# Optimization experiments

Hardware: AMD Instinct MI355X
Metric: run time of the kernel (lower is better)

The kernel has to match this reference:

```python
import jax, jax.numpy as jnp
import numpy as np

N_NODES = 100000
N_EDGES = 1600000
D = 64
PROP_STEP = 4
RESIDUAL = 1.0


def setup_inputs() -> dict:
    key = jax.random.key(0)
    ks = jax.random.split(key, 6)
    in_feat = jax.random.normal(ks[0], (N_NODES, D), dtype=jnp.float32)
    edge_weight = jax.random.uniform(ks[1], (N_EDGES,), dtype=jnp.float32)
    W1 = jax.random.normal(ks[2], (D, D), dtype=jnp.float32) / np.sqrt(D)
    b1 = jnp.zeros((D,), dtype=jnp.float32)
    W2 = jax.random.normal(ks[3], (D, D), dtype=jnp.float32) / np.sqrt(D)
    b2 = jnp.zeros((D,), dtype=jnp.float32)
    src = jax.random.randint(ks[4], (N_EDGES,), 0, N_NODES, dtype=jnp.int64 if jax.config.jax_enable_x64 else jnp.int32)
    dst = jax.random.randint(ks[5], (N_EDGES,), 0, N_NODES, dtype=jnp.int64 if jax.config.jax_enable_x64 else jnp.int32)
    return {"in_feat": in_feat, "edge_weight": edge_weight, "W1": W1, "b1": b1,
            "W2": W2, "b2": b2, "src": src, "dst": dst}


def _gcn_conv(x, W, b, src, dst, w):
    # GCNConv: out = A_hat @ (x W) + b, A_hat given as weighted edge list
    xw = x @ W                         # [N, D] dense GEMM (small D)
    msg = xw[src] * w[:, None]         # [E, D] gather + scale
    agg = jax.ops.segment_sum(msg, dst, num_segments=N_NODES)  # scatter-add
    return agg + b


def reference(in_feat, edge_weight, W1, b1, W2, b2, src, dst):
    ori = in_feat
    h = _gcn_conv(in_feat, W1, b1, src, dst, edge_weight) + RESIDUAL * ori
    for _ in range(1, PROP_STEP):
        h = _gcn_conv(h, W2, b2, src, dst, edge_weight) + RESIDUAL * ori
    return h
```

## Files before the change

### kernel.cpp

```cpp
#include <hip/hip_runtime.h>
#include <hip/hip_fp16.h>

#define NN 100000
#define NE 1600000
#define D 64
#define NPS 256
#define NS ((NN + NPS - 1) / NPS)
#define CAPS 4608
#define P1_BLOCKS 512
#define P1_CH (NE / P1_BLOCKS)

typedef __attribute__((ext_vector_type(8))) _Float16 half8;
typedef __attribute__((ext_vector_type(4))) _Float16 half4_t;
typedef __attribute__((ext_vector_type(4))) float f32x4;

__global__ void __launch_bounds__(256) gemm64_f32(const float* __restrict__ x,
                                                  const float* __restrict__ W,
                                                  __half* __restrict__ out,
                                                  __half* __restrict__ xh, int n) {
    __shared__ _Float16 sWT[64][72];
    int tid = threadIdx.x;
    for (int i = tid; i < 64 * 64; i += 256) {
        int k = i >> 6, c = i & 63;
        sWT[c][k] = (_Float16)W[i];
    }
    __syncthreads();
    int lane = tid & 63;
    int wid  = tid >> 6;
    int lrow = lane & 15;
    int kslc = lane >> 4;

    half8 bfrag[4][2];
#pragma unroll
    for (int t = 0; t < 4; ++t)
#pragma unroll
        for (int kb = 0; kb < 2; ++kb)
            bfrag[t][kb] = *(const half8*)&sWT[t * 16 + lrow][kb * 32 + kslc * 8];

    int nstrips = (n + 15) >> 4;
    for (int s = blockIdx.x * 4 + wid; s < nstrips; s += gridDim.x * 4) {
        int row = s * 16 + lrow;
        half8 a0 = {}, a1 = {};
        if (row < n) {
            const float* p = x + (size_t)row * 64 + kslc * 8;
            float4 u0 = *(const float4*)p;
            float4 u1 = *(const float4*)(p + 4);
            float4 u2 = *(const float4*)(p + 32);
            float4 u3 = *(const float4*)(p + 36);
            a0 = (half8){(_Float16)u0.x, (_Float16)u0.y, (_Float16)u0.z, (_Float16)u0.w,
                         (_Float16)u1.x, (_Float16)u1.y, (_Float16)u1.z, (_Float16)u1.w};
            a1 = (half8){(_Float16)u2.x, (_Float16)u2.y, (_Float16)u2.z, (_Float16)u2.w,
                         (_Float16)u3.x, (_Float16)u3.y, (_Float16)u3.z, (_Float16)u3.w};
            *(half8*)(xh + (size_t)row * 64 + kslc * 8) = a0;
            *(half8*)(xh + (size_t)row * 64 + 32 + kslc * 8) = a1;
        }
        f32x4 acc0 = {0.f, 0.f, 0.f, 0.f}, acc1 = acc0, acc2 = acc0, acc3 = acc0;
        acc0 = __builtin_amdgcn_mfma_f32_16x16x32_f16(a0, bfrag[0][0], acc0, 0, 0, 0);
        acc0 = __builtin_amdgcn_mfma_f32_16x16x32_f16(a1, bfrag[0][1], acc0, 0, 0, 0);
        acc1 = __builtin_amdgcn_mfma_f32_16x16x32_f16(a0, bfrag[1][0], acc1, 0, 0, 0);
        acc1 = __builtin_amdgcn_mfma_f32_16x16x32_f16(a1, bfrag[1][1], acc1, 0, 0, 0);
        acc2 = __builtin_amdgcn_mfma_f32_16x16x32_f16(a0, bfrag[2][0], acc2, 0, 0, 0);
        acc2 = __builtin_amdgcn_mfma_f32_16x16x32_f16(a1, bfrag[2][1], acc2, 0, 0, 0);
        acc3 = __builtin_amdgcn_mfma_f32_16x16x32_f16(a0, bfrag[3][0], acc3, 0, 0, 0);
        acc3 = __builtin_amdgcn_mfma_f32_16x16x32_f16(a1, bfrag[3][1], acc3, 0, 0, 0);

        int grow0 = s * 16 + kslc * 4;
#pragma unroll
        for (int j = 0; j < 4; ++j) {
            int grow = grow0 + j;
            if (grow < n) {
                __half* o = out + (size_t)grow * 64 + lrow;
                o[0]  = __float2half(acc0[j]);
                o[16] = __float2half(acc1[j]);
                o[32] = __float2half(acc2[j]);
                o[48] = __float2half(acc3[j]);
            }
        }
    }
}

__global__ void __launch_bounds__(256) gemm64_h(const __half* __restrict__ x,
                                                const float* __restrict__ W,
                                                __half* __restrict__ out, int n) {
    __shared__ _Float16 sWT[64][72];
    int tid = threadIdx.x;
    for (int i = tid; i < 64 * 64; i += 256) {
        int k = i >> 6, c = i & 63;
        sWT[c][k] = (_Float16)W[i];
    }
    __syncthreads();
    int lane = tid & 63;
    int wid  = tid >> 6;
    int lrow = lane & 15;
    int kslc = lane >> 4;

    half8 bfrag[4][2];
#pragma unroll
    for (int t = 0; t < 4; ++t)
#pragma unroll
        for (int kb = 0; kb < 2; ++kb)
            bfrag[t][kb] = *(const half8*)&sWT[t * 16 + lrow][kb * 32 + kslc * 8];

    int nstrips = (n + 15) >> 4;
    for (int s = blockIdx.x * 4 + wid; s < nstrips; s += gridDim.x * 4) {
        int row = s * 16 + lrow;
        half8 a0 = {}, a1 = {};
        if (row < n) {
            const __half* p = x + (size_t)row * 64 + kslc * 8;
            a0 = *(const half8*)p;
            a1 = *(const half8*)(p + 32);
        }
        f32x4 acc0 = {0.f, 0.f, 0.f, 0.f}, acc1 = acc0, acc2 = acc0, acc3 = acc0;
        acc0 = __builtin_amdgcn_mfma_f32_16x16x32_f16(a0, bfrag[0][0], acc0, 0, 0, 0);
        acc0 = __builtin_amdgcn_mfma_f32_16x16x32_f16(a1, bfrag[0][1], acc0, 0, 0, 0);
        acc1 = __builtin_amdgcn_mfma_f32_16x16x32_f16(a0, bfrag[1][0], acc1, 0, 0, 0);
        acc1 = __builtin_amdgcn_mfma_f32_16x16x32_f16(a1, bfrag[1][1], acc1, 0, 0, 0);
        acc2 = __builtin_amdgcn_mfma_f32_16x16x32_f16(a0, bfrag[2][0], acc2, 0, 0, 0);
        acc2 = __builtin_amdgcn_mfma_f32_16x16x32_f16(a1, bfrag[2][1], acc2, 0, 0, 0);
        acc3 = __builtin_amdgcn_mfma_f32_16x16x32_f16(a0, bfrag[3][0], acc3, 0, 0, 0);
        acc3 = __builtin_amdgcn_mfma_f32_16x16x32_f16(a1, bfrag[3][1], acc3, 0, 0, 0);

        int grow0 = s * 16 + kslc * 4;
#pragma unroll
        for (int j = 0; j < 4; ++j) {
            int grow = grow0 + j;
            if (grow < n) {
                __half* o = out + (size_t)grow * 64 + lrow;
                o[0]  = __float2half(acc0[j]);
                o[16] = __float2half(acc1[j]);
                o[32] = __float2half(acc2[j]);
                o[48] = __float2half(acc3[j]);
            }
        }
    }
}

__global__ void super_append(const int* __restrict__ src, const int* __restrict__ dst,
                             const float* __restrict__ w, int* __restrict__ scnt,
                             int2* __restrict__ tmp) {
    __shared__ int hist[NS];
    int tid = threadIdx.x;
    int e0 = blockIdx.x * P1_CH;
    int e1 = e0 + P1_CH;

    for (int t = tid; t < NS; t += blockDim.x) hist[t] = 0;
    __syncthreads();
    for (int e = e0 + tid; e < e1; e += blockDim.x)
        atomicAdd(&hist[dst[e] >> 8], 1);
    __syncthreads();
    for (int t = tid; t < NS; t += blockDim.x) {
        int h = hist[t];
        if (h) hist[t] = atomicAdd(&scnt[t], h);
    }
    __syncthreads();
    for (int e = e0 + tid; e < e1; e += blockDim.x) {
        int d = dst[e];
        int b = d >> 8;
        int p = atomicAdd(&hist[b], 1);
        if (p < CAPS) {
            int w0 = src[e] | ((d & (NPS - 1)) << 17);
            tmp[(size_t)b * CAPS + p] = make_int2(w0, __float_as_int(w[e]));
        }
    }
}

__global__ void scan_supers(const int* __restrict__ scnt, int* __restrict__ sbase,
                            int* __restrict__ offsets) {
    __shared__ int s[512];
    int t = threadIdx.x;
    int v = (t < NS) ? min(scnt[t], CAPS) : 0;
    s[t] = v;
    __syncthreads();
    for (int off = 1; off < 512; off <<= 1) {
        int x = (t >= off) ? s[t - off] : 0;
        __syncthreads();
        s[t] += x;
        __syncthreads();
    }
    if (t < NS) sbase[t] = s[t] - v;
    if (t == 511) offsets[NN] = s[511];
}

__global__ void super_sort(const int2* __restrict__ tmp, const int* __restrict__ scnt,
                           const int* __restrict__ sbase, int* __restrict__ offsets,
                           unsigned* __restrict__ sew) {
    __shared__ int hcnt[NPS];
    __shared__ int hoff[NPS];
    int b = blockIdx.x;
    int tid = threadIdx.x;
    int c = min(scnt[b], CAPS);
    const int2* in = tmp + (size_t)b * CAPS;

    hcnt[tid] = 0;
    __syncthreads();
    for (int i = tid; i < c; i += blockDim.x)
        atomicAdd(&hcnt[(in[i].x >> 17) & (NPS - 1)], 1);
    __syncthreads();
    int v = hcnt[tid];
    hoff[tid] = v;
    __syncthreads();
    for (int off = 1; off < NPS; off <<= 1) {
        int x = (tid >= off) ? hoff[tid - off] : 0;
        __syncthreads();
        hoff[tid] += x;
        __syncthreads();
    }
    int excl = hoff[tid] - v;
    int base = sbase[b];
    int gnode = b * NPS + tid;
    if (gnode < NN) offsets[gnode] = base + excl;
    hcnt[tid] = excl;
    __syncthreads();
    for (int i = tid; i < c; i += blockDim.x) {
        int2 e = in[i];
        int dl = (e.x >> 17) & (NPS - 1);
        int s = e.x & 0x1FFFF;
        float w = __int_as_float(e.y);
        int wq = __float2int_rn(w * 32768.f);
        if (wq > 32767) wq = 32767;
        int p = atomicAdd(&hcnt[dl], 1);
        sew[base + p] = (unsigned)s | ((unsigned)wq << 17);
    }
}

__global__ void pull_agg(const __half* __restrict__ xw, const unsigned* __restrict__ sew,
                         const int* __restrict__ offsets,
                         const __half* __restrict__ orih, const float* __restrict__ b,
                         __half* __restrict__ hout, float* __restrict__ fout, int n) {
    const float WS = 1.f / 32768.f;
    int tid = threadIdx.x;
    int lane = tid & 63;
    int g  = lane >> 4;
    int fl = lane & 15;
    int gwave = (int)((blockIdx.x * blockDim.x + tid) >> 6);
    int nw = (int)((gridDim.x * blockDim.x) >> 6);
    float4 bias = *(const float4*)&b[fl * 4];

    for (int v = gwave; v < n; v += nw) {
        int e0 = offsets[v];
        int e1 = offsets[v + 1];
        float ax = 0.f, ay = 0.f, az = 0.f, aw = 0.f;
        for (int base = e0; base < e1; base += 64) {
            int m = e1 - base;
            if (m > 64) m = 64;
            unsigned my = (lane < m) ? sew[base + lane] : 0u;
            int nit = (m + 3) >> 2;
            int j = 0;
            for (; j + 4 <= nit; j += 4) {
                unsigned p0 = __shfl(my, (j + 0) * 4 + g, 64);
                unsigned p1 = __shfl(my, (j + 1) * 4 + g, 64);
                unsigned p2 = __shfl(my, (j + 2) * 4 + g, 64);
                unsigned p3 = __shfl(my, (j + 3) * 4 + g, 64);
                half4_t h0 = *(const half4_t*)(xw + (size_t)(p0 & 0x1FFFF) * D + fl * 4);
                half4_t h1 = *(const half4_t*)(xw + (size_t)(p1 & 0x1FFFF) * D + fl * 4);
                half4_t h2 = *(const half4_t*)(xw + (size_t)(p2 & 0x1FFFF) * D + fl * 4);
                half4_t h3 = *(const half4_t*)(xw + (size_t)(p3 & 0x1FFFF) * D + fl * 4);
                float w0 = (float)(p0 >> 17) * WS;
                float w1 = (float)(p1 >> 17) * WS;
                float w2 = (float)(p2 >> 17) * WS;
                float w3 = (float)(p3 >> 17) * WS;
                ax = fmaf((float)h0.x, w0, ax); ay = fmaf((float)h0.y, w0, ay);
                az = fmaf((float)h0.z, w0, az); aw = fmaf((float)h0.w, w0, aw);
                ax = fmaf((float)h1.x, w1, ax); ay = fmaf((float)h1.y, w1, ay);
                az = fmaf((float)h1.z, w1, az); aw = fmaf((float)h1.w, w1, aw);
                ax = fmaf((float)h2.x, w2, ax); ay = fmaf((float)h2.y, w2, ay);
                az = fmaf((float)h2.z, w2, az); aw = fmaf((float)h2.w, w2, aw);
                ax = fmaf((float)h3.x, w3, ax); ay = fmaf((float)h3.y, w3, ay);
                az = fmaf((float)h3.z, w3, az); aw = fmaf((float)h3.w, w3, aw);
            }
            for (; j < nit; ++j) {
                unsigned p = __shfl(my, j * 4 + g, 64);
                half4_t h = *(const half4_t*)(xw + (size_t)(p & 0x1FFFF) * D + fl * 4);
                float wj = (float)(p >> 17) * WS;
                ax = fmaf((float)h.x, wj, ax); ay = fmaf((float)h.y, wj, ay);
                az = fmaf((float)h.z, wj, az); aw = fmaf((float)h.w, wj, aw);
            }
        }
        ax += __shfl_xor(ax, 16, 64); ax += __shfl_xor(ax, 32, 64);
        ay += __shfl_xor(ay, 16, 64); ay += __shfl_xor(ay, 32, 64);
        az += __shfl_xor(az, 16, 64); az += __shfl_xor(az, 32, 64);
        aw += __shfl_xor(aw, 16, 64); aw += __shfl_xor(aw, 32, 64);
        if (g == 0) {
            half4_t o4 = *(const half4_t*)(orih + (size_t)v * D + fl * 4);
            float rx = ax + bias.x + (float)o4.x;
            float ry = ay + bias.y + (float)o4.y;
            float rz = az + bias.z + (float)o4.z;
            float rw = aw + bias.w + (float)o4.w;
            if (fout) {
                float4 r = {rx, ry, rz, rw};
                *(float4*)&fout[(size_t)v * D + fl * 4] = r;
            } else {
                half4_t r = {(_Float16)rx, (_Float16)ry, (_Float16)rz, (_Float16)rw};
                *(half4_t*)&hout[(size_t)v * D + fl * 4] = r;
            }
        }
    }
}

extern "C" void kernel_launch(void* const* d_in, const int* in_sizes, int n_in,
                              void* d_out, int out_size, void* d_ws, size_t ws_size,
                              hipStream_t stream) {
    const float* in_feat = (const float*)d_in[0];
    const float* ew      = (const float*)d_in[1];
    const float* W1      = (const float*)d_in[2];
    const float* b1      = (const float*)d_in[3];
    const float* W2      = (const float*)d_in[4];
    const float* b2      = (const float*)d_in[5];
    const int*   src     = (const int*)d_in[6];
    const int*   dst     = (const int*)d_in[7];
    float* out = (float*)d_out;

    char* base = (char*)d_ws;
    int2*     tmp     = (int2*)base;
    __half*   hh      = (__half*)(base + (size_t)NS * CAPS * 8);
    __half*   xw      = hh + (size_t)NN * D;
    __half*   orih    = xw + (size_t)NN * D;
    unsigned* sew     = (unsigned*)(orih + (size_t)NN * D);
    int*      scnt    = (int*)(sew + NE);
    int*      sbase   = scnt + NS;
    int*      offsets = sbase + NS;

    hipMemsetAsync(scnt, 0, NS * sizeof(int), stream);
    super_append<<<P1_BLOCKS, 256, 0, stream>>>(src, dst, ew, scnt, tmp);
    scan_supers<<<1, 512, 0, stream>>>(scnt, sbase, offsets);
    super_sort<<<NS, 256, 0, stream>>>(tmp, scnt, sbase, offsets, sew);

    gemm64_f32<<<512, 256, 0, stream>>>(in_feat, W1, xw, orih, NN);
    pull_agg<<<4096, 256, 0, stream>>>(xw, sew, offsets, orih, b1, hh, nullptr, NN);

    for (int s = 0; s < 2; ++s) {
        gemm64_h<<<512, 256, 0, stream>>>(hh, W2, xw, NN);
        pull_agg<<<4096, 256, 0, stream>>>(xw, sew, offsets, orih, b2, hh, nullptr, NN);
    }

    gemm64_h<<<512, 256, 0, stream>>>(hh, W2, xw, NN);
    pull_agg<<<4096, 256, 0, stream>>>(xw, sew, offsets, orih, b2, nullptr, out, NN);
}
```

Measured before the change: 241.0 us.

## Stage edge bucketing and per-node sort in shared memory for coalesced writes

super_append now runs 256 blocks of 1024 threads. Each block computes local bucket offsets with a shared-memory scan and places its edges into LDS in bucket order before writing them to the global tmp buckets, so the scattered global stores become contiguous runs. super_sort uses 512 threads and builds the sorted per-bucket edge list in an LDS buffer, then copies it to sew with coalesced stores. The memset is replaced by a tiny zeroing kernel. The larger LDS footprint (about 57KB in super_append) limits occupancy, and the staging adds extra barriers.

```diff
diff --git a/kernel.cpp b/kernel.cpp
--- a/kernel.cpp
+++ b/kernel.cpp
@@ -7,7 +7,8 @@
 #define NPS 256
 #define NS ((NN + NPS - 1) / NPS)
 #define CAPS 4608
-#define P1_BLOCKS 512
+#define P1_BLOCKS 256
+#define P1_T 1024
 #define P1_CH (NE / P1_BLOCKS)
 
 typedef __attribute__((ext_vector_type(8))) _Float16 half8;
@@ -135,32 +136,58 @@
     }
 }
 
-__global__ void super_append(const int* __restrict__ src, const int* __restrict__ dst,
-                             const float* __restrict__ w, int* __restrict__ scnt,
-                             int2* __restrict__ tmp) {
+__global__ void zero_scnt(int* __restrict__ scnt) {
+    int t = threadIdx.x;
+    if (t < NS) scnt[t] = 0;
+}
+
+__global__ void __launch_bounds__(P1_T) super_append(
+        const int* __restrict__ src, const int* __restrict__ dst,
+        const float* __restrict__ w, int* __restrict__ scnt,
+        int2* __restrict__ tmp) {
     __shared__ int hist[NS];
+    __shared__ int loff[512];
+    __shared__ int gres[NS];
+    __shared__ int slotL[P1_CH];
+    __shared__ int2 payL[P1_CH];
     int tid = threadIdx.x;
     int e0 = blockIdx.x * P1_CH;
     int e1 = e0 + P1_CH;
 
-    for (int t = tid; t < NS; t += blockDim.x) hist[t] = 0;
-    __syncthreads();
-    for (int e = e0 + tid; e < e1; e += blockDim.x)
+    for (int t = tid; t < NS; t += P1_T) hist[t] = 0;
+    __syncthreads();
+    for (int e = e0 + tid; e < e1; e += P1_T)
         atomicAdd(&hist[dst[e] >> 8], 1);
     __syncthreads();
-    for (int t = tid; t < NS; t += blockDim.x) {
-        int h = hist[t];
-        if (h) hist[t] = atomicAdd(&scnt[t], h);
-    }
-    __syncthreads();
-    for (int e = e0 + tid; e < e1; e += blockDim.x) {
+    if (tid < 512) loff[tid] = (tid < NS) ? hist[tid] : 0;
+    __syncthreads();
+    for (int off = 1; off < 512; off <<= 1) {
+        int x = (tid < 512 && tid >= off) ? loff[tid - off] : 0;
+        __syncthreads();
+        if (tid < 512) loff[tid] += x;
+        __syncthreads();
+    }
+    if (tid < NS) {
+        int h = hist[tid];
+        gres[tid] = h ? atomicAdd(&scnt[tid], h) : 0;
+        loff[tid] -= h;
+        hist[tid] = 0;
+    }
+    __syncthreads();
+    for (int e = e0 + tid; e < e1; e += P1_T) {
         int d = dst[e];
-        int b = d >> 8;
-        int p = atomicAdd(&hist[b], 1);
-        if (p < CAPS) {
-            int w0 = src[e] | ((d & (NPS - 1)) << 17);
-            tmp[(size_t)b * CAPS + p] = make_int2(w0, __float_as_int(w[e]));
-        }
+        int s = d >> 8;
+        int r = atomicAdd(&hist[s], 1);
+        int p = loff[s] + r;
+        int g = gres[s] + r;
+        int w0 = src[e] | ((d & (NPS - 1)) << 17);
+        payL[p] = make_int2(w0, __float_as_int(w[e]));
+        slotL[p] = (g < CAPS) ? (s * CAPS + g) : -1;
+    }
+    __syncthreads();
+    for (int p = tid; p < P1_CH; p += P1_T) {
+        int g = slotL[p];
+        if (g >= 0) tmp[g] = payL[p];
     }
 }
 
@@ -181,46 +208,52 @@
     if (t == 511) offsets[NN] = s[511];
 }
 
-__global__ void super_sort(const int2* __restrict__ tmp, const int* __restrict__ scnt,
-                           const int* __restrict__ sbase, int* __restrict__ offsets,
-                           unsigned* __restrict__ sew) {
+__global__ void __launch_bounds__(512) super_sort(
+        const int2* __restrict__ tmp, const int* __restrict__ scnt,
+        const int* __restrict__ sbase, int* __restrict__ offsets,
+        unsigned* __restrict__ sew) {
     __shared__ int hcnt[NPS];
     __shared__ int hoff[NPS];
+    __shared__ unsigned pay[CAPS];
     int b = blockIdx.x;
     int tid = threadIdx.x;
     int c = min(scnt[b], CAPS);
     const int2* in = tmp + (size_t)b * CAPS;
 
-    hcnt[tid] = 0;
-    __syncthreads();
-    for (int i = tid; i < c; i += blockDim.x)
+    if (tid < NPS) hcnt[tid] = 0;
+    __syncthreads();
+    for (int i = tid; i < c; i += 512)
         atomicAdd(&hcnt[(in[i].x >> 17) & (NPS - 1)], 1);
     __syncthreads();
-    int v = hcnt[tid];
-    hoff[tid] = v;
+    if (tid < NPS) hoff[tid] = hcnt[tid];
     __syncthreads();
     for (int off = 1; off < NPS; off <<= 1) {
-        int x = (tid >= off) ? hoff[tid - off] : 0;
-        __syncthreads();
-        hoff[tid] += x;
-        __syncthreads();
-    }
-    int excl = hoff[tid] - v;
+        int x = (tid < NPS && tid >= off) ? hoff[tid - off] : 0;
+        __syncthreads();
+        if (tid < NPS) hoff[tid] += x;
+        __syncthreads();
+    }
     int base = sbase[b];
-    int gnode = b * NPS + tid;
-    if (gnode < NN) offsets[gnode] = base + excl;
-    hcnt[tid] = excl;
-    __syncthreads();
-    for (int i = tid; i < c; i += blockDim.x) {
+    if (tid < NPS) {
+        int ex = hoff[tid] - hcnt[tid];
+        int gnode = b * NPS + tid;
+        if (gnode < NN) offsets[gnode] = base + ex;
+        hoff[tid] = ex;
+        hcnt[tid] = 0;
+    }
+    __syncthreads();
+    for (int i = tid; i < c; i += 512) {
         int2 e = in[i];
         int dl = (e.x >> 17) & (NPS - 1);
         int s = e.x & 0x1FFFF;
-        float w = __int_as_float(e.y);
-        int wq = __float2int_rn(w * 32768.f);
+        float wv = __int_as_float(e.y);
+        int wq = __float2int_rn(wv * 32768.f);
         if (wq > 32767) wq = 32767;
-        int p = atomicAdd(&hcnt[dl], 1);
-        sew[base + p] = (unsigned)s | ((unsigned)wq << 17);
-    }
+        int r = atomicAdd(&hcnt[dl], 1);
+        pay[hoff[dl] + r] = (unsigned)s | ((unsigned)wq << 17);
+    }
+    __syncthreads();
+    for (int i = tid; i < c; i += 512) sew[base + i] = pay[i];
 }
 
 __global__ void pull_agg(const __half* __restrict__ xw, const unsigned* __restrict__ sew,
@@ -320,10 +353,10 @@
     int*      sbase   = scnt + NS;
     int*      offsets = sbase + NS;
 
-    hipMemsetAsync(scnt, 0, NS * sizeof(int), stream);
-    super_append<<<P1_BLOCKS, 256, 0, stream>>>(src, dst, ew, scnt, tmp);
+    zero_scnt<<<1, 512, 0, stream>>>(scnt);
+    super_append<<<P1_BLOCKS, P1_T, 0, stream>>>(src, dst, ew, scnt, tmp);
     scan_supers<<<1, 512, 0, stream>>>(scnt, sbase, offsets);
-    super_sort<<<NS, 256, 0, stream>>>(tmp, scnt, sbase, offsets, sew);
+    super_sort<<<NS, 512, 0, stream>>>(tmp, scnt, sbase, offsets, sew);
 
     gemm64_f32<<<512, 256, 0, stream>>>(in_feat, W1, xw, orih, NN);
     pull_agg<<<4096, 256, 0, stream>>>(xw, sew, offsets, orih, b1, hh, nullptr, NN);
```

Measured after the change: 219.5 us (median of 2 runs). 1.1x faster.
